# Kernel optimization log

Measured on AMD Instinct MI355X. Metric: run time of the kernel, lower is better.

## Reference

```python
import jax, jax.numpy as jnp
import numpy as np

B, NQ, NK, D, H, DK, DV, M = 1, 2048, 2048, 1024, 16, 64, 64, 64
EPS = 1e-5

def _layer_norm(x, gamma, beta):
    mu = jnp.mean(x, axis=-1, keepdims=True)
    var = jnp.mean(jnp.square(x - mu), axis=-1, keepdims=True)
    return (x - mu) * jax.lax.rsqrt(var + EPS) * gamma + beta

def setup_inputs() -> dict:
    key = jax.random.key(0)
    ks = jax.random.split(key, 16)
    s = 0.02  # xavier-ish init scale for 1024x1024 weights
    return {
        'queries': jax.random.normal(ks[0], (B, NQ, D), jnp.float32),
        'keys': jax.random.normal(ks[1], (B, NK, D), jnp.float32),
        'values': jax.random.normal(ks[2], (B, NK, D), jnp.float32),
        'attention_weights': jax.random.uniform(ks[3], (B, NQ, NK), jnp.float32),
        'prev_att': jax.random.normal(ks[4], (B, NQ, NK), jnp.float32) * 0.1,
        'attention_mask': jax.random.randint(ks[5], (B, NQ, NK), 0, 2).astype(bool),
        'Wq': jax.random.normal(ks[6], (H * DK, D), jnp.float32) * s,
        'bq': jnp.zeros((H * DK,), jnp.float32),
        'Wk': jax.random.normal(ks[7], (H * DK, D), jnp.float32) * s,
        'bk': jnp.zeros((H * DK,), jnp.float32),
        'Wv': jax.random.normal(ks[8], (H * DV, D), jnp.float32) * s,
        'bv': jnp.zeros((H * DV,), jnp.float32),
        'Wo': jax.random.normal(ks[9], (D, H * DV), jnp.float32) * s,
        'bo': jnp.zeros((D,), jnp.float32),
        'm_k': jax.random.normal(ks[10], (1, H, DK, M), jnp.float32) * s,  # stored pre-permuted as in module
        'm_v': jax.random.normal(ks[11], (1, H, M, DV), jnp.float32) * s,
        'gamma': jnp.ones((D,), jnp.float32),
        'beta': jnp.zeros((D,), jnp.float32),
    }

def reference(queries, keys, values, attention_weights, prev_att, attention_mask,
              Wq, bq, Wk, bk, Wv, bv, Wo, bo, m_k, m_v, gamma, beta):
    b, nq = queries.shape[:2]
    nk = keys.shape[1]
    # projections -> (b, h, nq, dk), (b, h, dk, nk), (b, h, nk, dv)
    q = (queries @ Wq.T + bq).reshape(b, nq, H, DK).transpose(0, 2, 1, 3)
    k = (keys @ Wk.T + bk).reshape(b, nk, H, DK).transpose(0, 2, 3, 1)
    v = (values @ Wv.T + bv).reshape(b, nk, H, DV).transpose(0, 2, 1, 3)
    # memory-slot concatenation
    k = jnp.concatenate([k, jnp.broadcast_to(m_k, (b, H, DK, M))], axis=3)   # (b,h,dk,nk+M)
    v = jnp.concatenate([v, jnp.broadcast_to(m_v, (b, H, M, DV))], axis=2)   # (b,h,nk+M,dv)
    aw = jnp.concatenate([attention_weights, jnp.ones((b, nq, M), attention_weights.dtype)], axis=-1)
    pa = jnp.concatenate([prev_att, jnp.zeros((b, nq, M), prev_att.dtype)], axis=-1)
    mask = jnp.concatenate([attention_mask, jnp.zeros((b, nq, M), bool)], axis=-1)
    # scores: scale, reweight, bias, mask (b_s==1 so rank-3 aw/pa broadcast over heads as in torch)
    att = jnp.einsum('bhqd,bhdn->bhqn', q, k) / np.sqrt(DK).astype(np.float32)
    att = att * aw + pa
    r_att = jnp.where(mask[:, None, :, :], -jnp.inf, att)
    p = jax.nn.softmax(r_att, axis=-1)  # dropout is identity (p=0 / eval)
    out = jnp.einsum('bhqn,bhnv->bqhv', p, v).reshape(b, nq, H * DV)
    out = out @ Wo.T + bo
    out = _layer_norm(queries + out, gamma, beta)  # use_res=True
    return out, r_att
```

## Files before the change

kernel.cpp:

```cpp
#include <hip/hip_runtime.h>
#include <math.h>

#define NQ 2048
#define NK 2048
#define DMODEL 1024
#define NHEAD 16
#define DK 64
#define DV 64
#define MSLOT 64
#define NKM (NK + MSLOT)
#define OUT_ELEMS (NQ * DMODEL)

#define NEG_BIG (-1.0e30f)

#define LD4(p) (*(const float4*)(p))
#define ST4(p, v) (*(float4*)(p) = (v))

using bfx8 = __attribute__((ext_vector_type(8))) short;
using fx4  = __attribute__((ext_vector_type(4))) float;

static __device__ __forceinline__ unsigned short f2bf(float f) {
    union { float f; unsigned u; } v; v.f = f;
    unsigned r = v.u + 0x7fffu + ((v.u >> 16) & 1u);
    return (unsigned short)(r >> 16);
}
static __device__ __forceinline__ float bf2f(unsigned short u) {
    union { unsigned u; float f; } v; v.u = (unsigned)u << 16;
    return v.f;
}

__global__ __launch_bounds__(256) void qkv_gemm(
    const float* __restrict__ Xq, const float* __restrict__ Xk, const float* __restrict__ Xv,
    const float* __restrict__ Wq, const float* __restrict__ Wk, const float* __restrict__ Wv,
    const float* __restrict__ bq, const float* __restrict__ bk, const float* __restrict__ bv,
    unsigned short* __restrict__ Qb, unsigned short* __restrict__ Kb,
    unsigned short* __restrict__ Vb)
{
    const int z = blockIdx.z;
    const float* X = (z == 0) ? Xq : (z == 1) ? Xk : Xv;
    const float* W = (z == 0) ? Wq : (z == 1) ? Wk : Wv;
    const float* bias = (z == 0) ? bq : (z == 1) ? bk : bv;
    unsigned short* O = (z == 0) ? Qb : (z == 1) ? Kb : Vb;

    __shared__ float Xs[32][68];
    __shared__ float Ws[32][68];
    const int t = threadIdx.x;
    const int ty = t >> 4, tx = t & 15;
    const int m0 = blockIdx.y * 64, n0 = blockIdx.x * 64;
    const int K = DMODEL;
    float acc[4][4] = {};

    const int u = (t < 128) ? t : (t - 128);
    const int r4 = (u >> 3) * 4;
    const int c4 = u & 7;
    const float* src = (t < 128) ? &X[(size_t)(m0 + r4) * K + c4 * 4]
                                 : &W[(size_t)(n0 + r4) * K + c4 * 4];

    float4 v0 = LD4(src), v1 = LD4(src + K), v2 = LD4(src + 2 * K), v3 = LD4(src + 3 * K);

    for (int k0 = 0; k0 < K; k0 += 32) {
        __syncthreads();
        if (t < 128) {
            ST4(&Xs[c4 * 4 + 0][r4], make_float4(v0.x, v1.x, v2.x, v3.x));
            ST4(&Xs[c4 * 4 + 1][r4], make_float4(v0.y, v1.y, v2.y, v3.y));
            ST4(&Xs[c4 * 4 + 2][r4], make_float4(v0.z, v1.z, v2.z, v3.z));
            ST4(&Xs[c4 * 4 + 3][r4], make_float4(v0.w, v1.w, v2.w, v3.w));
        } else {
            ST4(&Ws[c4 * 4 + 0][r4], make_float4(v0.x, v1.x, v2.x, v3.x));
            ST4(&Ws[c4 * 4 + 1][r4], make_float4(v0.y, v1.y, v2.y, v3.y));
            ST4(&Ws[c4 * 4 + 2][r4], make_float4(v0.z, v1.z, v2.z, v3.z));
            ST4(&Ws[c4 * 4 + 3][r4], make_float4(v0.w, v1.w, v2.w, v3.w));
        }
        if (k0 + 32 < K) {
            const float* p = src + k0 + 32;
            v0 = LD4(p); v1 = LD4(p + K); v2 = LD4(p + 2 * K); v3 = LD4(p + 3 * K);
        }
        __syncthreads();
#pragma unroll 8
        for (int kk = 0; kk < 32; ++kk) {
            float a[4], b[4];
            *(float4*)&a[0] = LD4(&Xs[kk][ty * 4]);
            *(float4*)&b[0] = LD4(&Ws[kk][tx * 4]);
#pragma unroll
            for (int i = 0; i < 4; ++i)
#pragma unroll
                for (int j = 0; j < 4; ++j)
                    acc[i][j] += a[i] * b[j];
        }
    }
    float4 bv4 = LD4(&bias[n0 + tx * 4]);
#pragma unroll
    for (int i = 0; i < 4; ++i) {
        ushort4 o;
        o.x = f2bf(acc[i][0] + bv4.x);
        o.y = f2bf(acc[i][1] + bv4.y);
        o.z = f2bf(acc[i][2] + bv4.z);
        o.w = f2bf(acc[i][3] + bv4.w);
        *(ushort4*)(O + (size_t)(m0 + ty * 4 + i) * DMODEL + n0 + tx * 4) = o;
    }
}

__global__ __launch_bounds__(256) void vt_prep(
    const unsigned short* __restrict__ Vb, const float* __restrict__ mv,
    unsigned short* __restrict__ Vt)
{
    __shared__ unsigned short L[64][72];
    const int c = blockIdx.x;
    const int h = blockIdx.y;
    const int t = threadIdx.x;
    const int rn = t >> 2;
    const int g4 = t & 3;

    if (c < 32) {
        const unsigned short* p = Vb + (size_t)(c * 64 + rn) * DMODEL + h * DV + g4 * 16;
#pragma unroll
        for (int e = 0; e < 16; ++e) L[rn][g4 * 16 + e] = p[e];
    } else {
        const float* p = mv + ((size_t)h * MSLOT + rn) * DV + g4 * 16;
#pragma unroll
        for (int e = 0; e < 16; ++e) L[rn][g4 * 16 + e] = f2bf(p[e]);
    }
    __syncthreads();
    const int dv = rn;
    unsigned short* q = Vt + ((size_t)h * DV + dv) * NKM + c * 64 + g4 * 16;
#pragma unroll
    for (int e = 0; e < 16; ++e) q[e] = L[g4 * 16 + e][dv];
}

__global__ __launch_bounds__(256) void scores_mfma(
    const unsigned short* __restrict__ Qb, const unsigned short* __restrict__ Kb,
    const float* __restrict__ AW, const float* __restrict__ PA,
    const unsigned char* __restrict__ MASK, float* __restrict__ Ratt,
    float2* __restrict__ pf)
{
    const int t = threadIdx.x;
    const int lane = t & 63, w = t >> 6;
    const int wq = w >> 1, wn = w & 1;
    const int h = blockIdx.z;
    const int q0 = blockIdx.y * 128, n0 = blockIdx.x * 128;
    const int lr = lane & 15, lg = lane >> 4;

    const unsigned short* qbase = Qb + (size_t)(q0 + wq * 64 + lr) * DMODEL + h * DK + lg * 8;
    const unsigned short* kbase = Kb + (size_t)(n0 + wn * 64 + lr) * DMODEL + h * DK + lg * 8;

    fx4 acc[4][4] = {};
#pragma unroll
    for (int kt = 0; kt < 2; ++kt) {
        bfx8 a[4], b[4];
#pragma unroll
        for (int mt = 0; mt < 4; ++mt) a[mt] = *(const bfx8*)(qbase + mt * 16 * DMODEL + kt * 32);
#pragma unroll
        for (int nt = 0; nt < 4; ++nt) b[nt] = *(const bfx8*)(kbase + nt * 16 * DMODEL + kt * 32);
#pragma unroll
        for (int mt = 0; mt < 4; ++mt)
#pragma unroll
            for (int nt = 0; nt < 4; ++nt)
                acc[mt][nt] = __builtin_amdgcn_mfma_f32_16x16x32_bf16(a[mt], b[nt], acc[mt][nt], 0, 0, 0);
    }

#pragma unroll
    for (int mt = 0; mt < 4; ++mt) {
#pragma unroll
        for (int reg = 0; reg < 4; ++reg) {
            const int q = q0 + wq * 64 + mt * 16 + lg * 4 + reg;
            const size_t awb = (size_t)q * NK + n0 + wn * 64 + lr;
            const size_t rb  = ((size_t)h * NQ + q) * NKM + n0 + wn * 64 + lr;
            float o[4];
#pragma unroll
            for (int nt = 0; nt < 4; ++nt) {
                float s = acc[mt][nt][reg] * 0.125f;
                float aw = AW[awb + nt * 16];
                float pa = PA[awb + nt * 16];
                unsigned char mm = MASK[awb + nt * 16];
                o[nt] = mm ? NEG_BIG : fmaf(s, aw, pa);
                Ratt[rb + nt * 16] = o[nt];
            }
            float m = fmaxf(fmaxf(o[0], o[1]), fmaxf(o[2], o[3]));
#pragma unroll
            for (int x = 8; x >= 1; x >>= 1) m = fmaxf(m, __shfl_xor(m, x));
            float s = expf(o[0] - m) + expf(o[1] - m) + expf(o[2] - m) + expf(o[3] - m);
#pragma unroll
            for (int x = 8; x >= 1; x >>= 1) s += __shfl_xor(s, x);
            if (lr == 0)
                pf[((size_t)h * NQ + q) * 33 + blockIdx.x * 2 + wn] = make_float2(m, s);
        }
    }
}

__global__ __launch_bounds__(256) void scores_mem(
    const unsigned short* __restrict__ Qb, const float* __restrict__ mk,
    float* __restrict__ Ratt, float2* __restrict__ pf)
{
    __shared__ float Qs[64][132];
    __shared__ float Ks[64][68];
    const int t = threadIdx.x;
    const int h = blockIdx.y;
    const int q0 = blockIdx.x * 128;

#pragma unroll
    for (int i = 0; i < 4; ++i) {
        int idx = t + i * 256;
        int row = idx >> 3, g = idx & 7;
        const unsigned short* p = Qb + (size_t)(q0 + row) * DMODEL + h * DK + g * 8;
#pragma unroll
        for (int e = 0; e < 8; ++e) Qs[g * 8 + e][row] = bf2f(p[e]);
    }
#pragma unroll
    for (int i = 0; i < 4; ++i) {
        int idx = t + i * 256;
        int dk = idx >> 4, c4 = idx & 15;
        ST4(&Ks[dk][c4 * 4], LD4(&mk[((size_t)h * DK + dk) * MSLOT + c4 * 4]));
    }
    __syncthreads();

    const int ty = t >> 4, tx = t & 15;
    float acc[8][4] = {};
#pragma unroll 4
    for (int kk = 0; kk < 64; ++kk) {
        float a[8], b[4];
        *(float4*)&a[0] = LD4(&Qs[kk][ty * 8]);
        *(float4*)&a[4] = LD4(&Qs[kk][ty * 8 + 4]);
        *(float4*)&b[0] = LD4(&Ks[kk][tx * 4]);
#pragma unroll
        for (int i = 0; i < 8; ++i)
#pragma unroll
            for (int j = 0; j < 4; ++j)
                acc[i][j] += a[i] * b[j];
    }
#pragma unroll
    for (int i = 0; i < 8; ++i) {
        int q = q0 + ty * 8 + i;
        float o0 = acc[i][0] * 0.125f, o1 = acc[i][1] * 0.125f;
        float o2 = acc[i][2] * 0.125f, o3 = acc[i][3] * 0.125f;
        ST4(&Ratt[((size_t)h * NQ + q) * NKM + NK + tx * 4], make_float4(o0, o1, o2, o3));
        float m = fmaxf(fmaxf(o0, o1), fmaxf(o2, o3));
#pragma unroll
        for (int x = 8; x >= 1; x >>= 1) m = fmaxf(m, __shfl_xor(m, x));
        float s = expf(o0 - m) + expf(o1 - m) + expf(o2 - m) + expf(o3 - m);
#pragma unroll
        for (int x = 8; x >= 1; x >>= 1) s += __shfl_xor(s, x);
        if (tx == 0)
            pf[((size_t)h * NQ + q) * 33 + 32] = make_float2(m, s);
    }
}

__global__ __launch_bounds__(256) void stats_reduce(
    const float2* __restrict__ pf, float* __restrict__ stats)
{
    const int w = threadIdx.x >> 6, lane = threadIdx.x & 63;
    const int row = blockIdx.x * 4 + w;
    float m = NEG_BIG, s = 0.f;
    if (lane < 33) { float2 p = pf[(size_t)row * 33 + lane]; m = p.x; s = p.y; }
    float M = m;
#pragma unroll
    for (int x = 32; x >= 1; x >>= 1) M = fmaxf(M, __shfl_xor(M, x));
    float sc = s * expf(m - M);
#pragma unroll
    for (int x = 32; x >= 1; x >>= 1) sc += __shfl_xor(sc, x);
    if (lane == 0) { stats[row * 2] = M; stats[row * 2 + 1] = 1.f / sc; }
}

__global__ __launch_bounds__(256) void pv_mfma(
    const float* __restrict__ Ratt, const float* __restrict__ stats,
    const unsigned short* __restrict__ Vt, float* __restrict__ AO)
{
    const int t = threadIdx.x;
    const int lane = t & 63, w = t >> 6;
    const int h = blockIdx.y;
    const int q0 = blockIdx.x * 64 + w * 16;
    const int lr = lane & 15, lg = lane >> 4;

    const size_t srow = (size_t)h * NQ + q0 + lr;
    const float sm = stats[srow * 2];
    const float si = stats[srow * 2 + 1];
    const float* rp = Ratt + srow * NKM + lg * 8;
    const unsigned short* vb = Vt + ((size_t)h * DV + lr) * NKM + lg * 8;

    fx4 acc[4] = {};
#pragma unroll 2
    for (int kc = 0; kc < NKM; kc += 32) {
        float4 r0 = LD4(rp + kc), r1 = LD4(rp + kc + 4);
        union { unsigned short u[8]; bfx8 v; } P;
        P.u[0] = f2bf(expf(r0.x - sm) * si);
        P.u[1] = f2bf(expf(r0.y - sm) * si);
        P.u[2] = f2bf(expf(r0.z - sm) * si);
        P.u[3] = f2bf(expf(r0.w - sm) * si);
        P.u[4] = f2bf(expf(r1.x - sm) * si);
        P.u[5] = f2bf(expf(r1.y - sm) * si);
        P.u[6] = f2bf(expf(r1.z - sm) * si);
        P.u[7] = f2bf(expf(r1.w - sm) * si);
        bfx8 b0 = *(const bfx8*)(vb + kc);
        bfx8 b1 = *(const bfx8*)(vb + 16 * NKM + kc);
        bfx8 b2 = *(const bfx8*)(vb + 32 * NKM + kc);
        bfx8 b3 = *(const bfx8*)(vb + 48 * NKM + kc);
        acc[0] = __builtin_amdgcn_mfma_f32_16x16x32_bf16(P.v, b0, acc[0], 0, 0, 0);
        acc[1] = __builtin_amdgcn_mfma_f32_16x16x32_bf16(P.v, b1, acc[1], 0, 0, 0);
        acc[2] = __builtin_amdgcn_mfma_f32_16x16x32_bf16(P.v, b2, acc[2], 0, 0, 0);
        acc[3] = __builtin_amdgcn_mfma_f32_16x16x32_bf16(P.v, b3, acc[3], 0, 0, 0);
    }
#pragma unroll
    for (int nt = 0; nt < 4; ++nt)
#pragma unroll
        for (int reg = 0; reg < 4; ++reg)
            AO[(size_t)(q0 + lg * 4 + reg) * DMODEL + h * DV + nt * 16 + lr] = acc[nt][reg];
}

__global__ __launch_bounds__(256) void gemm64(
    const float* __restrict__ X, const float* __restrict__ W,
    const float* __restrict__ bias, float* __restrict__ C,
    int M, int N, int K)
{
    __shared__ float Xs[32][68];
    __shared__ float Ws[32][68];
    const int t = threadIdx.x;
    const int ty = t >> 4, tx = t & 15;
    const int m0 = blockIdx.y * 64, n0 = blockIdx.x * 64;
    float acc[4][4] = {};

    const int u = (t < 128) ? t : (t - 128);
    const int r4 = (u >> 3) * 4;
    const int c4 = u & 7;
    const float* src = (t < 128) ? &X[(size_t)(m0 + r4) * K + c4 * 4]
                                 : &W[(size_t)(n0 + r4) * K + c4 * 4];

    float4 v0 = LD4(src), v1 = LD4(src + K), v2 = LD4(src + 2 * K), v3 = LD4(src + 3 * K);

    for (int k0 = 0; k0 < K; k0 += 32) {
        __syncthreads();
        if (t < 128) {
            ST4(&Xs[c4 * 4 + 0][r4], make_float4(v0.x, v1.x, v2.x, v3.x));
            ST4(&Xs[c4 * 4 + 1][r4], make_float4(v0.y, v1.y, v2.y, v3.y));
            ST4(&Xs[c4 * 4 + 2][r4], make_float4(v0.z, v1.z, v2.z, v3.z));
            ST4(&Xs[c4 * 4 + 3][r4], make_float4(v0.w, v1.w, v2.w, v3.w));
        } else {
            ST4(&Ws[c4 * 4 + 0][r4], make_float4(v0.x, v1.x, v2.x, v3.x));
            ST4(&Ws[c4 * 4 + 1][r4], make_float4(v0.y, v1.y, v2.y, v3.y));
            ST4(&Ws[c4 * 4 + 2][r4], make_float4(v0.z, v1.z, v2.z, v3.z));
            ST4(&Ws[c4 * 4 + 3][r4], make_float4(v0.w, v1.w, v2.w, v3.w));
        }
        if (k0 + 32 < K) {
            const float* p = src + k0 + 32;
            v0 = LD4(p); v1 = LD4(p + K); v2 = LD4(p + 2 * K); v3 = LD4(p + 3 * K);
        }
        __syncthreads();
#pragma unroll 8
        for (int kk = 0; kk < 32; ++kk) {
            float a[4], b[4];
            *(float4*)&a[0] = LD4(&Xs[kk][ty * 4]);
            *(float4*)&b[0] = LD4(&Ws[kk][tx * 4]);
#pragma unroll
            for (int i = 0; i < 4; ++i)
#pragma unroll
                for (int j = 0; j < 4; ++j)
                    acc[i][j] += a[i] * b[j];
        }
    }
    float4 bv = LD4(&bias[n0 + tx * 4]);
#pragma unroll
    for (int i = 0; i < 4; ++i) {
        float4 o = make_float4(acc[i][0] + bv.x, acc[i][1] + bv.y,
                               acc[i][2] + bv.z, acc[i][3] + bv.w);
        ST4(&C[(size_t)(m0 + ty * 4 + i) * N + n0 + tx * 4], o);
    }
}

__global__ __launch_bounds__(256) void ln_kernel(
    const float* __restrict__ Xres, const float* __restrict__ T,
    const float* __restrict__ gamma, const float* __restrict__ beta,
    float* __restrict__ out)
{
    const int row = blockIdx.x;
    const int t = threadIdx.x;
    const int w = t >> 6, lane = t & 63;
    __shared__ float red1[4], red2[4];

    float4 x = LD4(&Xres[(size_t)row * DMODEL + t * 4]);
    float4 tv = LD4(&T[(size_t)row * DMODEL + t * 4]);
    float v0 = x.x + tv.x, v1 = x.y + tv.y, v2 = x.z + tv.z, v3 = x.w + tv.w;

    float s = v0 + v1 + v2 + v3;
#pragma unroll
    for (int o = 32; o > 0; o >>= 1) s += __shfl_xor(s, o);
    if (lane == 0) red1[w] = s;
    __syncthreads();
    float mu = (red1[0] + red1[1] + red1[2] + red1[3]) * (1.f / DMODEL);

    float d0 = v0 - mu, d1 = v1 - mu, d2 = v2 - mu, d3 = v3 - mu;
    float vs = d0 * d0 + d1 * d1 + d2 * d2 + d3 * d3;
#pragma unroll
    for (int o = 32; o > 0; o >>= 1) vs += __shfl_xor(vs, o);
    if (lane == 0) red2[w] = vs;
    __syncthreads();
    float inv = rsqrtf((red2[0] + red2[1] + red2[2] + red2[3]) * (1.f / DMODEL) + 1e-5f);

    float4 g = LD4(&gamma[t * 4]);
    float4 bb = LD4(&beta[t * 4]);
    float4 o4 = make_float4(d0 * inv * g.x + bb.x, d1 * inv * g.y + bb.y,
                            d2 * inv * g.z + bb.z, d3 * inv * g.w + bb.w);
    ST4(&out[(size_t)row * DMODEL + t * 4], o4);
}

extern "C" void kernel_launch(void* const* d_in, const int* in_sizes, int n_in,
                              void* d_out, int out_size, void* d_ws, size_t ws_size,
                              hipStream_t stream) {
    const float* queries = (const float*)d_in[0];
    const float* keys    = (const float*)d_in[1];
    const float* values  = (const float*)d_in[2];
    const float* AW      = (const float*)d_in[3];
    const float* PA      = (const float*)d_in[4];
    const unsigned char* MASK = (const unsigned char*)d_in[5];
    const float* Wq = (const float*)d_in[6];  const float* bq = (const float*)d_in[7];
    const float* Wk = (const float*)d_in[8];  const float* bk = (const float*)d_in[9];
    const float* Wv = (const float*)d_in[10]; const float* bv = (const float*)d_in[11];
    const float* Wo = (const float*)d_in[12]; const float* bo = (const float*)d_in[13];
    const float* mk = (const float*)d_in[14]; const float* mv = (const float*)d_in[15];
    const float* gamma = (const float*)d_in[16]; const float* beta = (const float*)d_in[17];

    float* out  = (float*)d_out;
    float* ratt = out + OUT_ELEMS;

    char* base = (char*)d_ws;
    unsigned short* Qb = (unsigned short*)(base);
    unsigned short* Kb = (unsigned short*)(base + (4u << 20));
    unsigned short* Vb = (unsigned short*)(base + (8u << 20));
    unsigned short* Vt = (unsigned short*)(base + (12u << 20));
    float* AO    = (float*)(base + 16908288);
    float* T     = (float*)(base + 25296896);
    float* stats = (float*)(base + 33685504);
    float2* pf   = (float2*)AO;

    qkv_gemm<<<dim3(DMODEL / 64, NQ / 64, 3), 256, 0, stream>>>(
        queries, keys, values, Wq, Wk, Wv, bq, bk, bv, Qb, Kb, Vb);

    vt_prep<<<dim3(33, NHEAD), 256, 0, stream>>>(Vb, mv, Vt);

    scores_mfma<<<dim3(NK / 128, NQ / 128, NHEAD), 256, 0, stream>>>(
        Qb, Kb, AW, PA, MASK, ratt, pf);

    scores_mem<<<dim3(NQ / 128, NHEAD), 256, 0, stream>>>(Qb, mk, ratt, pf);

    stats_reduce<<<(NHEAD * NQ) / 4, 256, 0, stream>>>(pf, stats);

    pv_mfma<<<dim3(NQ / 64, NHEAD), 256, 0, stream>>>(ratt, stats, Vt, AO);

    gemm64<<<dim3(DMODEL / 64, NQ / 64), 256, 0, stream>>>(
        AO, Wo, bo, T, NQ, DMODEL, DMODEL);

    ln_kernel<<<NQ, 256, 0, stream>>>(queries, T, gamma, beta, out);
}
```

Before: 924.7 us.

## Use bf16 MFMA for projection GEMMs and vectorize score epilogue

Converts inputs and weights to bf16 in a pre-pass and replaces the FP32 SIMT QKV and output-projection GEMMs with MFMA-based kernels. The scores kernel swaps operand roles so each lane handles 4 contiguous columns, enabling float4 loads of weights/bias and packed mask reads. The PV kernel stages score tiles in shared memory and writes the attention output in bf16. Extra conversion traffic and reduced precision in the output projection are the trade-offs.

```diff
diff --git a/kernel.cpp b/kernel.cpp
--- a/kernel.cpp
+++ b/kernel.cpp
@@ -29,75 +29,100 @@
     return v.f;
 }
 
-__global__ __launch_bounds__(256) void qkv_gemm(
-    const float* __restrict__ Xq, const float* __restrict__ Xk, const float* __restrict__ Xv,
-    const float* __restrict__ Wq, const float* __restrict__ Wk, const float* __restrict__ Wv,
+__global__ __launch_bounds__(256) void conv_bf16(
+    const float* __restrict__ q, const float* __restrict__ k, const float* __restrict__ v,
+    const float* __restrict__ wq, const float* __restrict__ wk, const float* __restrict__ wv,
+    const float* __restrict__ wo,
+    unsigned short* __restrict__ xq, unsigned short* __restrict__ xk, unsigned short* __restrict__ xv,
+    unsigned short* __restrict__ bwq, unsigned short* __restrict__ bwk,
+    unsigned short* __restrict__ bwv, unsigned short* __restrict__ bwo)
+{
+    const int seg = blockIdx.y;
+    const float* s; unsigned short* d; int n;
+    switch (seg) {
+        case 0: s = q;  d = xq;  n = 2097152; break;
+        case 1: s = k;  d = xk;  n = 2097152; break;
+        case 2: s = v;  d = xv;  n = 2097152; break;
+        case 3: s = wq; d = bwq; n = 1048576; break;
+        case 4: s = wk; d = bwk; n = 1048576; break;
+        case 5: s = wv; d = bwv; n = 1048576; break;
+        default: s = wo; d = bwo; n = 1048576; break;
+    }
+    int i = (blockIdx.x * 256 + threadIdx.x) * 8;
+    if (i >= n) return;
+    float4 a = LD4(s + i), b = LD4(s + i + 4);
+    ushort4 o0 = { f2bf(a.x), f2bf(a.y), f2bf(a.z), f2bf(a.w) };
+    ushort4 o1 = { f2bf(b.x), f2bf(b.y), f2bf(b.z), f2bf(b.w) };
+    *(ushort4*)(d + i) = o0;
+    *(ushort4*)(d + i + 4) = o1;
+}
+
+template<bool FP32OUT>
+static __device__ __forceinline__ void gemm_mfma_body(
+    const unsigned short* __restrict__ X, const unsigned short* __restrict__ W,
+    const float* __restrict__ bias, void* __restrict__ C, int m0, int n0)
+{
+    const int t = threadIdx.x;
+    const int lane = t & 63, w = t >> 6;
+    const int wm = w >> 1, wn = w & 1;
+    const int lr = lane & 15, lg = lane >> 4;
+
+    const unsigned short* xb = X + (size_t)(m0 + wm * 32 + lr) * DMODEL + lg * 8;
+    const unsigned short* wb = W + (size_t)(n0 + wn * 32 + lr) * DMODEL + lg * 8;
+
+    fx4 acc[2][2] = {};
+#pragma unroll 4
+    for (int kt = 0; kt < 32; ++kt) {
+        bfx8 a0 = *(const bfx8*)(wb + kt * 32);
+        bfx8 a1 = *(const bfx8*)(wb + 16 * DMODEL + kt * 32);
+        bfx8 b0 = *(const bfx8*)(xb + kt * 32);
+        bfx8 b1 = *(const bfx8*)(xb + 16 * DMODEL + kt * 32);
+        acc[0][0] = __builtin_amdgcn_mfma_f32_16x16x32_bf16(a0, b0, acc[0][0], 0, 0, 0);
+        acc[0][1] = __builtin_amdgcn_mfma_f32_16x16x32_bf16(a0, b1, acc[0][1], 0, 0, 0);
+        acc[1][0] = __builtin_amdgcn_mfma_f32_16x16x32_bf16(a1, b0, acc[1][0], 0, 0, 0);
+        acc[1][1] = __builtin_amdgcn_mfma_f32_16x16x32_bf16(a1, b1, acc[1][1], 0, 0, 0);
+    }
+#pragma unroll
+    for (int nt = 0; nt < 2; ++nt) {
+#pragma unroll
+        for (int mt = 0; mt < 2; ++mt) {
+            const int m = m0 + wm * 32 + mt * 16 + lr;
+            const int n = n0 + wn * 32 + nt * 16 + lg * 4;
+            float4 bv = LD4(&bias[n]);
+            float r0 = acc[nt][mt][0] + bv.x, r1 = acc[nt][mt][1] + bv.y;
+            float r2 = acc[nt][mt][2] + bv.z, r3 = acc[nt][mt][3] + bv.w;
+            if (FP32OUT) {
+                ST4(&((float*)C)[(size_t)m * DMODEL + n], make_float4(r0, r1, r2, r3));
+            } else {
+                ushort4 o = { f2bf(r0), f2bf(r1), f2bf(r2), f2bf(r3) };
+                *(ushort4*)((unsigned short*)C + (size_t)m * DMODEL + n) = o;
+            }
+        }
+    }
+}
+
+__global__ __launch_bounds__(256) void qkv_mfma(
+    const unsigned short* __restrict__ Xq, const unsigned short* __restrict__ Xk,
+    const unsigned short* __restrict__ Xv,
+    const unsigned short* __restrict__ Wq, const unsigned short* __restrict__ Wk,
+    const unsigned short* __restrict__ Wv,
     const float* __restrict__ bq, const float* __restrict__ bk, const float* __restrict__ bv,
     unsigned short* __restrict__ Qb, unsigned short* __restrict__ Kb,
     unsigned short* __restrict__ Vb)
 {
     const int z = blockIdx.z;
-    const float* X = (z == 0) ? Xq : (z == 1) ? Xk : Xv;
-    const float* W = (z == 0) ? Wq : (z == 1) ? Wk : Wv;
-    const float* bias = (z == 0) ? bq : (z == 1) ? bk : bv;
+    const unsigned short* X = (z == 0) ? Xq : (z == 1) ? Xk : Xv;
+    const unsigned short* W = (z == 0) ? Wq : (z == 1) ? Wk : Wv;
+    const float* b = (z == 0) ? bq : (z == 1) ? bk : bv;
     unsigned short* O = (z == 0) ? Qb : (z == 1) ? Kb : Vb;
-
-    __shared__ float Xs[32][68];
-    __shared__ float Ws[32][68];
-    const int t = threadIdx.x;
-    const int ty = t >> 4, tx = t & 15;
-    const int m0 = blockIdx.y * 64, n0 = blockIdx.x * 64;
-    const int K = DMODEL;
-    float acc[4][4] = {};
-
-    const int u = (t < 128) ? t : (t - 128);
-    const int r4 = (u >> 3) * 4;
-    const int c4 = u & 7;
-    const float* src = (t < 128) ? &X[(size_t)(m0 + r4) * K + c4 * 4]
-                                 : &W[(size_t)(n0 + r4) * K + c4 * 4];
-
-    float4 v0 = LD4(src), v1 = LD4(src + K), v2 = LD4(src + 2 * K), v3 = LD4(src + 3 * K);
-
-    for (int k0 = 0; k0 < K; k0 += 32) {
-        __syncthreads();
-        if (t < 128) {
-            ST4(&Xs[c4 * 4 + 0][r4], make_float4(v0.x, v1.x, v2.x, v3.x));
-            ST4(&Xs[c4 * 4 + 1][r4], make_float4(v0.y, v1.y, v2.y, v3.y));
-            ST4(&Xs[c4 * 4 + 2][r4], make_float4(v0.z, v1.z, v2.z, v3.z));
-            ST4(&Xs[c4 * 4 + 3][r4], make_float4(v0.w, v1.w, v2.w, v3.w));
-        } else {
-            ST4(&Ws[c4 * 4 + 0][r4], make_float4(v0.x, v1.x, v2.x, v3.x));
-            ST4(&Ws[c4 * 4 + 1][r4], make_float4(v0.y, v1.y, v2.y, v3.y));
-            ST4(&Ws[c4 * 4 + 2][r4], make_float4(v0.z, v1.z, v2.z, v3.z));
-            ST4(&Ws[c4 * 4 + 3][r4], make_float4(v0.w, v1.w, v2.w, v3.w));
-        }
-        if (k0 + 32 < K) {
-            const float* p = src + k0 + 32;
-            v0 = LD4(p); v1 = LD4(p + K); v2 = LD4(p + 2 * K); v3 = LD4(p + 3 * K);
-        }
-        __syncthreads();
-#pragma unroll 8
-        for (int kk = 0; kk < 32; ++kk) {
-            float a[4], b[4];
-            *(float4*)&a[0] = LD4(&Xs[kk][ty * 4]);
-            *(float4*)&b[0] = LD4(&Ws[kk][tx * 4]);
-#pragma unroll
-            for (int i = 0; i < 4; ++i)
-#pragma unroll
-                for (int j = 0; j < 4; ++j)
-                    acc[i][j] += a[i] * b[j];
-        }
-    }
-    float4 bv4 = LD4(&bias[n0 + tx * 4]);
-#pragma unroll
-    for (int i = 0; i < 4; ++i) {
-        ushort4 o;
-        o.x = f2bf(acc[i][0] + bv4.x);
-        o.y = f2bf(acc[i][1] + bv4.y);
-        o.z = f2bf(acc[i][2] + bv4.z);
-        o.w = f2bf(acc[i][3] + bv4.w);
-        *(ushort4*)(O + (size_t)(m0 + ty * 4 + i) * DMODEL + n0 + tx * 4) = o;
-    }
+    gemm_mfma_body<false>(X, W, b, O, blockIdx.y * 64, blockIdx.x * 64);
+}
+
+__global__ __launch_bounds__(256) void oproj_mfma(
+    const unsigned short* __restrict__ AOb, const unsigned short* __restrict__ Wob,
+    const float* __restrict__ bo, float* __restrict__ T)
+{
+    gemm_mfma_body<true>(AOb, Wob, bo, T, blockIdx.y * 64, blockIdx.x * 64);
 }
 
 __global__ __launch_bounds__(256) void vt_prep(
@@ -140,50 +165,55 @@
     const int q0 = blockIdx.y * 128, n0 = blockIdx.x * 128;
     const int lr = lane & 15, lg = lane >> 4;
 
+    const unsigned short* kbase = Kb + (size_t)(n0 + wn * 64 + lr) * DMODEL + h * DK + lg * 8;
     const unsigned short* qbase = Qb + (size_t)(q0 + wq * 64 + lr) * DMODEL + h * DK + lg * 8;
-    const unsigned short* kbase = Kb + (size_t)(n0 + wn * 64 + lr) * DMODEL + h * DK + lg * 8;
 
     fx4 acc[4][4] = {};
 #pragma unroll
     for (int kt = 0; kt < 2; ++kt) {
         bfx8 a[4], b[4];
 #pragma unroll
-        for (int mt = 0; mt < 4; ++mt) a[mt] = *(const bfx8*)(qbase + mt * 16 * DMODEL + kt * 32);
-#pragma unroll
-        for (int nt = 0; nt < 4; ++nt) b[nt] = *(const bfx8*)(kbase + nt * 16 * DMODEL + kt * 32);
-#pragma unroll
-        for (int mt = 0; mt < 4; ++mt)
-#pragma unroll
-            for (int nt = 0; nt < 4; ++nt)
-                acc[mt][nt] = __builtin_amdgcn_mfma_f32_16x16x32_bf16(a[mt], b[nt], acc[mt][nt], 0, 0, 0);
-    }
-
-#pragma unroll
-    for (int mt = 0; mt < 4; ++mt) {
-#pragma unroll
-        for (int reg = 0; reg < 4; ++reg) {
-            const int q = q0 + wq * 64 + mt * 16 + lg * 4 + reg;
-            const size_t awb = (size_t)q * NK + n0 + wn * 64 + lr;
-            const size_t rb  = ((size_t)h * NQ + q) * NKM + n0 + wn * 64 + lr;
-            float o[4];
-#pragma unroll
-            for (int nt = 0; nt < 4; ++nt) {
-                float s = acc[mt][nt][reg] * 0.125f;
-                float aw = AW[awb + nt * 16];
-                float pa = PA[awb + nt * 16];
-                unsigned char mm = MASK[awb + nt * 16];
-                o[nt] = mm ? NEG_BIG : fmaf(s, aw, pa);
-                Ratt[rb + nt * 16] = o[nt];
-            }
-            float m = fmaxf(fmaxf(o[0], o[1]), fmaxf(o[2], o[3]));
-#pragma unroll
-            for (int x = 8; x >= 1; x >>= 1) m = fmaxf(m, __shfl_xor(m, x));
-            float s = expf(o[0] - m) + expf(o[1] - m) + expf(o[2] - m) + expf(o[3] - m);
-#pragma unroll
-            for (int x = 8; x >= 1; x >>= 1) s += __shfl_xor(s, x);
-            if (lr == 0)
-                pf[((size_t)h * NQ + q) * 33 + blockIdx.x * 2 + wn] = make_float2(m, s);
+        for (int nt = 0; nt < 4; ++nt) a[nt] = *(const bfx8*)(kbase + nt * 16 * DMODEL + kt * 32);
+#pragma unroll
+        for (int qt = 0; qt < 4; ++qt) b[qt] = *(const bfx8*)(qbase + qt * 16 * DMODEL + kt * 32);
+#pragma unroll
+        for (int nt = 0; nt < 4; ++nt)
+#pragma unroll
+            for (int qt = 0; qt < 4; ++qt)
+                acc[nt][qt] = __builtin_amdgcn_mfma_f32_16x16x32_bf16(a[nt], b[qt], acc[nt][qt], 0, 0, 0);
+    }
+
+    const int nb = n0 + wn * 64 + lg * 4;
+#pragma unroll
+    for (int qt = 0; qt < 4; ++qt) {
+        const int q = q0 + wq * 64 + qt * 16 + lr;
+        const size_t mrow = (size_t)q * NK;
+        const size_t rrow = ((size_t)h * NQ + q) * NKM;
+        float o[4][4];
+        float m = NEG_BIG;
+#pragma unroll
+        for (int nt = 0; nt < 4; ++nt) {
+            const int n = nb + nt * 16;
+            float4 aw = LD4(&AW[mrow + n]);
+            float4 pa = LD4(&PA[mrow + n]);
+            unsigned mm = *(const unsigned*)(MASK + mrow + n);
+            o[nt][0] = (mm & 0x000000ffu) ? NEG_BIG : fmaf(acc[nt][qt][0] * 0.125f, aw.x, pa.x);
+            o[nt][1] = (mm & 0x0000ff00u) ? NEG_BIG : fmaf(acc[nt][qt][1] * 0.125f, aw.y, pa.y);
+            o[nt][2] = (mm & 0x00ff0000u) ? NEG_BIG : fmaf(acc[nt][qt][2] * 0.125f, aw.z, pa.z);
+            o[nt][3] = (mm & 0xff000000u) ? NEG_BIG : fmaf(acc[nt][qt][3] * 0.125f, aw.w, pa.w);
+            ST4(&Ratt[rrow + n], make_float4(o[nt][0], o[nt][1], o[nt][2], o[nt][3]));
+            m = fmaxf(m, fmaxf(fmaxf(o[nt][0], o[nt][1]), fmaxf(o[nt][2], o[nt][3])));
         }
+        m = fmaxf(m, __shfl_xor(m, 16));
+        m = fmaxf(m, __shfl_xor(m, 32));
+        float s = 0.f;
+#pragma unroll
+        for (int nt = 0; nt < 4; ++nt)
+            s += expf(o[nt][0] - m) + expf(o[nt][1] - m) + expf(o[nt][2] - m) + expf(o[nt][3] - m);
+        s += __shfl_xor(s, 16);
+        s += __shfl_xor(s, 32);
+        if (lg == 0)
+            pf[((size_t)h * NQ + q) * 33 + blockIdx.x * 2 + wn] = make_float2(m, s);
     }
 }
 
@@ -262,106 +292,68 @@
 
 __global__ __launch_bounds__(256) void pv_mfma(
     const float* __restrict__ Ratt, const float* __restrict__ stats,
-    const unsigned short* __restrict__ Vt, float* __restrict__ AO)
-{
+    const unsigned short* __restrict__ Vt, unsigned short* __restrict__ AOb)
+{
+    __shared__ float Ps[64][68];
     const int t = threadIdx.x;
     const int lane = t & 63, w = t >> 6;
     const int h = blockIdx.y;
-    const int q0 = blockIdx.x * 64 + w * 16;
+    const int q0 = blockIdx.x * 64;
     const int lr = lane & 15, lg = lane >> 4;
 
-    const size_t srow = (size_t)h * NQ + q0 + lr;
+    const size_t srow = (size_t)h * NQ + q0 + w * 16 + lr;
     const float sm = stats[srow * 2];
     const float si = stats[srow * 2 + 1];
-    const float* rp = Ratt + srow * NKM + lg * 8;
-    const unsigned short* vb = Vt + ((size_t)h * DV + lr) * NKM + lg * 8;
+    const unsigned short* vbase = Vt + ((size_t)h * DV + lr) * NKM;
+    const float* rbase = Ratt + ((size_t)h * NQ + q0) * NKM;
+
+    const int strow = t >> 4;
+    const int stcol = (t & 15) * 4;
 
     fx4 acc[4] = {};
-#pragma unroll 2
-    for (int kc = 0; kc < NKM; kc += 32) {
-        float4 r0 = LD4(rp + kc), r1 = LD4(rp + kc + 4);
-        union { unsigned short u[8]; bfx8 v; } P;
-        P.u[0] = f2bf(expf(r0.x - sm) * si);
-        P.u[1] = f2bf(expf(r0.y - sm) * si);
-        P.u[2] = f2bf(expf(r0.z - sm) * si);
-        P.u[3] = f2bf(expf(r0.w - sm) * si);
-        P.u[4] = f2bf(expf(r1.x - sm) * si);
-        P.u[5] = f2bf(expf(r1.y - sm) * si);
-        P.u[6] = f2bf(expf(r1.z - sm) * si);
-        P.u[7] = f2bf(expf(r1.w - sm) * si);
-        bfx8 b0 = *(const bfx8*)(vb + kc);
-        bfx8 b1 = *(const bfx8*)(vb + 16 * NKM + kc);
-        bfx8 b2 = *(const bfx8*)(vb + 32 * NKM + kc);
-        bfx8 b3 = *(const bfx8*)(vb + 48 * NKM + kc);
-        acc[0] = __builtin_amdgcn_mfma_f32_16x16x32_bf16(P.v, b0, acc[0], 0, 0, 0);
-        acc[1] = __builtin_amdgcn_mfma_f32_16x16x32_bf16(P.v, b1, acc[1], 0, 0, 0);
-        acc[2] = __builtin_amdgcn_mfma_f32_16x16x32_bf16(P.v, b2, acc[2], 0, 0, 0);
-        acc[3] = __builtin_amdgcn_mfma_f32_16x16x32_bf16(P.v, b3, acc[3], 0, 0, 0);
+    for (int tile = 0; tile < 33; ++tile) {
+        const int kc = tile * 64;
+        float4 s0 = LD4(rbase + (size_t)(strow +  0) * NKM + kc + stcol);
+        float4 s1 = LD4(rbase + (size_t)(strow + 16) * NKM + kc + stcol);
+        float4 s2 = LD4(rbase + (size_t)(strow + 32) * NKM + kc + stcol);
+        float4 s3 = LD4(rbase + (size_t)(strow + 48) * NKM + kc + stcol);
+        __syncthreads();
+        ST4(&Ps[strow][stcol], s0);
+        ST4(&Ps[strow + 16][stcol], s1);
+        ST4(&Ps[strow + 32][stcol], s2);
+        ST4(&Ps[strow + 48][stcol], s3);
+        __syncthreads();
+#pragma unroll
+        for (int half = 0; half < 2; ++half) {
+            const int nb = half * 32 + lg * 8;
+            float4 r0 = LD4(&Ps[w * 16 + lr][nb]);
+            float4 r1 = LD4(&Ps[w * 16 + lr][nb + 4]);
+            union { unsigned short u[8]; bfx8 v; } P;
+            P.u[0] = f2bf(expf(r0.x - sm) * si);
+            P.u[1] = f2bf(expf(r0.y - sm) * si);
+            P.u[2] = f2bf(expf(r0.z - sm) * si);
+            P.u[3] = f2bf(expf(r0.w - sm) * si);
+            P.u[4] = f2bf(expf(r1.x - sm) * si);
+            P.u[5] = f2bf(expf(r1.y - sm) * si);
+            P.u[6] = f2bf(expf(r1.z - sm) * si);
+            P.u[7] = f2bf(expf(r1.w - sm) * si);
+            const unsigned short* vk = vbase + kc + nb;
+            bfx8 b0 = *(const bfx8*)(vk);
+            bfx8 b1 = *(const bfx8*)(vk + 16 * NKM);
+            bfx8 b2 = *(const bfx8*)(vk + 32 * NKM);
+            bfx8 b3 = *(const bfx8*)(vk + 48 * NKM);
+            acc[0] = __builtin_amdgcn_mfma_f32_16x16x32_bf16(P.v, b0, acc[0], 0, 0, 0);
+            acc[1] = __builtin_amdgcn_mfma_f32_16x16x32_bf16(P.v, b1, acc[1], 0, 0, 0);
+            acc[2] = __builtin_amdgcn_mfma_f32_16x16x32_bf16(P.v, b2, acc[2], 0, 0, 0);
+            acc[3] = __builtin_amdgcn_mfma_f32_16x16x32_bf16(P.v, b3, acc[3], 0, 0, 0);
+        }
     }
 #pragma unroll
     for (int nt = 0; nt < 4; ++nt)
 #pragma unroll
         for (int reg = 0; reg < 4; ++reg)
-            AO[(size_t)(q0 + lg * 4 + reg) * DMODEL + h * DV + nt * 16 + lr] = acc[nt][reg];
-}
-
-__global__ __launch_bounds__(256) void gemm64(
-    const float* __restrict__ X, const float* __restrict__ W,
-    const float* __restrict__ bias, float* __restrict__ C,
-    int M, int N, int K)
-{
-    __shared__ float Xs[32][68];
-    __shared__ float Ws[32][68];
-    const int t = threadIdx.x;
-    const int ty = t >> 4, tx = t & 15;
-    const int m0 = blockIdx.y * 64, n0 = blockIdx.x * 64;
-    float acc[4][4] = {};
-
-    const int u = (t < 128) ? t : (t - 128);
-    const int r4 = (u >> 3) * 4;
-    const int c4 = u & 7;
-    const float* src = (t < 128) ? &X[(size_t)(m0 + r4) * K + c4 * 4]
-                                 : &W[(size_t)(n0 + r4) * K + c4 * 4];
-
-    float4 v0 = LD4(src), v1 = LD4(src + K), v2 = LD4(src + 2 * K), v3 = LD4(src + 3 * K);
-
-    for (int k0 = 0; k0 < K; k0 += 32) {
-        __syncthreads();
-        if (t < 128) {
-            ST4(&Xs[c4 * 4 + 0][r4], make_float4(v0.x, v1.x, v2.x, v3.x));
-            ST4(&Xs[c4 * 4 + 1][r4], make_float4(v0.y, v1.y, v2.y, v3.y));
-            ST4(&Xs[c4 * 4 + 2][r4], make_float4(v0.z, v1.z, v2.z, v3.z));
-            ST4(&Xs[c4 * 4 + 3][r4], make_float4(v0.w, v1.w, v2.w, v3.w));
-        } else {
-            ST4(&Ws[c4 * 4 + 0][r4], make_float4(v0.x, v1.x, v2.x, v3.x));
-            ST4(&Ws[c4 * 4 + 1][r4], make_float4(v0.y, v1.y, v2.y, v3.y));
-            ST4(&Ws[c4 * 4 + 2][r4], make_float4(v0.z, v1.z, v2.z, v3.z));
-            ST4(&Ws[c4 * 4 + 3][r4], make_float4(v0.w, v1.w, v2.w, v3.w));
-        }
-        if (k0 + 32 < K) {
-            const float* p = src + k0 + 32;
-            v0 = LD4(p); v1 = LD4(p + K); v2 = LD4(p + 2 * K); v3 = LD4(p + 3 * K);
-        }
-        __syncthreads();
-#pragma unroll 8
-        for (int kk = 0; kk < 32; ++kk) {
-            float a[4], b[4];
-            *(float4*)&a[0] = LD4(&Xs[kk][ty * 4]);
-            *(float4*)&b[0] = LD4(&Ws[kk][tx * 4]);
-#pragma unroll
-            for (int i = 0; i < 4; ++i)
-#pragma unroll
-                for (int j = 0; j < 4; ++j)
-                    acc[i][j] += a[i] * b[j];
-        }
-    }
-    float4 bv = LD4(&bias[n0 + tx * 4]);
-#pragma unroll
-    for (int i = 0; i < 4; ++i) {
-        float4 o = make_float4(acc[i][0] + bv.x, acc[i][1] + bv.y,
-                               acc[i][2] + bv.z, acc[i][3] + bv.w);
-        ST4(&C[(size_t)(m0 + ty * 4 + i) * N + n0 + tx * 4], o);
-    }
+            AOb[(size_t)(q0 + w * 16 + lg * 4 + reg) * DMODEL + h * DV + nt * 16 + lr]
+                = f2bf(acc[nt][reg]);
 }
 
 __global__ __launch_bounds__(256) void ln_kernel(
@@ -419,18 +411,30 @@
     float* out  = (float*)d_out;
     float* ratt = out + OUT_ELEMS;
 
+    const size_t MB = 1u << 20;
     char* base = (char*)d_ws;
-    unsigned short* Qb = (unsigned short*)(base);
-    unsigned short* Kb = (unsigned short*)(base + (4u << 20));
-    unsigned short* Vb = (unsigned short*)(base + (8u << 20));
-    unsigned short* Vt = (unsigned short*)(base + (12u << 20));
-    float* AO    = (float*)(base + 16908288);
-    float* T     = (float*)(base + 25296896);
-    float* stats = (float*)(base + 33685504);
-    float2* pf   = (float2*)AO;
-
-    qkv_gemm<<<dim3(DMODEL / 64, NQ / 64, 3), 256, 0, stream>>>(
-        queries, keys, values, Wq, Wk, Wv, bq, bk, bv, Qb, Kb, Vb);
+    unsigned short* Xqb = (unsigned short*)(base);
+    unsigned short* Xkb = (unsigned short*)(base + 4 * MB);
+    unsigned short* Xvb = (unsigned short*)(base + 8 * MB);
+    unsigned short* Wqb = (unsigned short*)(base + 12 * MB);
+    unsigned short* Wkb = (unsigned short*)(base + 14 * MB);
+    unsigned short* Wvb = (unsigned short*)(base + 16 * MB);
+    unsigned short* Wob = (unsigned short*)(base + 18 * MB);
+    unsigned short* Qb  = (unsigned short*)(base + 20 * MB);
+    unsigned short* Kb  = (unsigned short*)(base + 24 * MB);
+    unsigned short* Vb  = (unsigned short*)(base + 28 * MB);
+    unsigned short* Vt  = (unsigned short*)(base + 32 * MB);
+    float*  T     = (float*)(base);
+    float2* pf    = (float2*)(base + 8 * MB);
+    float*  stats = (float*)(base + 17 * MB);
+    unsigned short* AOb = Qb;
+
+    conv_bf16<<<dim3(1024, 7), 256, 0, stream>>>(
+        queries, keys, values, Wq, Wk, Wv, Wo,
+        Xqb, Xkb, Xvb, Wqb, Wkb, Wvb, Wob);
+
+    qkv_mfma<<<dim3(DMODEL / 64, NQ / 64, 3), 256, 0, stream>>>(
+        Xqb, Xkb, Xvb, Wqb, Wkb, Wvb, bq, bk, bv, Qb, Kb, Vb);
 
     vt_prep<<<dim3(33, NHEAD), 256, 0, stream>>>(Vb, mv, Vt);
 
@@ -441,10 +445,9 @@
 
     stats_reduce<<<(NHEAD * NQ) / 4, 256, 0, stream>>>(pf, stats);
 
-    pv_mfma<<<dim3(NQ / 64, NHEAD), 256, 0, stream>>>(ratt, stats, Vt, AO);
-
-    gemm64<<<dim3(DMODEL / 64, NQ / 64), 256, 0, stream>>>(
-        AO, Wo, bo, T, NQ, DMODEL, DMODEL);
+    pv_mfma<<<dim3(NQ / 64, NHEAD), 256, 0, stream>>>(ratt, stats, Vt, AOb);
+
+    oproj_mfma<<<dim3(DMODEL / 64, NQ / 64), 256, 0, stream>>>(AOb, Wob, bo, T);
 
     ln_kernel<<<NQ, 256, 0, stream>>>(queries, T, gamma, beta, out);
 }
```

Result: faster. 762.0 us (-17.6%).
